# Optimization experiments

Measured on AMD Instinct MI355X. Metric: run time of the kernel, lower is better.

The kernel has to match this reference:

```python
import jax, jax.numpy as jnp
import numpy as np

P = 262144
H = 256
EPS = 1e-12  # torch F.normalize eps


def _l2norm(x):
    # matches torch.nn.functional.normalize(x, dim=-1): x / max(||x||, eps)
    n = jnp.linalg.norm(x, axis=-1, keepdims=True)
    return x / jnp.maximum(n, EPS)


def _mlp(x, params):
    # params: list of (W, b); ReLU on all but last layer
    for W, b in params[:-1]:
        x = jax.nn.relu(x @ W + b)
    W, b = params[-1]
    return x @ W + b


def setup_inputs() -> dict:
    key = jax.random.key(0)
    ks = jax.random.split(key, 24)
    inp = {
        "normals": jax.random.normal(ks[0], (P, 3), dtype=jnp.float32),
        "view_dirs": jax.random.normal(ks[1], (P, 3), dtype=jnp.float32),
        "roughness": jax.random.uniform(ks[2], (P, 1), dtype=jnp.float32),
        "r0": jax.random.uniform(ks[3], (P, 1), dtype=jnp.float32),
    }
    # diffuse MLP: 3 -> 256 -> 256 -> 256 -> 3
    d_dims = [3, H, H, H, 3]
    # specular MLP: 8 -> 256 -> 256 -> 256 -> 3
    s_dims = [8, H, H, H, 3]
    k = 4
    for i in range(4):
        fan = d_dims[i]
        inp[f"dW{i}"] = jax.random.normal(ks[k], (d_dims[i], d_dims[i + 1]), dtype=jnp.float32) * (2.0 / fan) ** 0.5
        inp[f"db{i}"] = jnp.zeros((d_dims[i + 1],), dtype=jnp.float32)
        k += 1
    for i in range(4):
        fan = s_dims[i]
        inp[f"sW{i}"] = jax.random.normal(ks[k], (s_dims[i], s_dims[i + 1]), dtype=jnp.float32) * (2.0 / fan) ** 0.5
        inp[f"sb{i}"] = jnp.zeros((s_dims[i + 1],), dtype=jnp.float32)
        k += 1
    return inp


def reference(normals, view_dirs, roughness, r0,
              dW0, db0, dW1, db1, dW2, db2, dW3, db3,
              sW0, sb0, sW1, sb1, sW2, sb2, sW3, sb3):
    n = _l2norm(normals)
    v = _l2norm(view_dirs)
    inputs_specular = jnp.concatenate((n, v, roughness, r0), axis=-1)  # [P,8]
    visible = (n * v).sum(axis=-1) > 0  # [P]
    d_params = [(dW0, db0), (dW1, db1), (dW2, db2), (dW3, db3)]
    s_params = [(sW0, sb0), (sW1, sb1), (sW2, sb2), (sW3, sb3)]
    # Faithful to gather->MLP->scatter-into-zeros: pointwise MLP computed
    # everywhere, non-visible rows zeroed (identical math, static shapes).
    mask = visible[:, None]
    diffuse_rgb = jnp.where(mask, _mlp(n, d_params), 0.0)
    specular_rgb = jnp.where(mask, _mlp(inputs_specular, s_params), 0.0)
    return (diffuse_rgb, specular_rgb)
```

## Files before the change

### kernel.cpp

```cpp
#include <hip/hip_runtime.h>

typedef _Float16 f16;
typedef _Float16 f16x8 __attribute__((ext_vector_type(8)));
typedef __fp16   fp16x2 __attribute__((ext_vector_type(2)));
typedef float    f32x16 __attribute__((ext_vector_type(16)));
typedef float    f32x4  __attribute__((ext_vector_type(4)));
typedef unsigned int u32;
typedef unsigned int u32x4 __attribute__((ext_vector_type(4)));

#define NPTS 262144

#define NET_F16   143360
#define L1_OFF    4096
#define L2_OFF    69632
#define L3_OFF    135168
#define BIAS_BYTE 573440
#define NCHUNK    70

static __device__ __forceinline__ u32 pkrtz(float a, float b) {
    fp16x2 h = __builtin_amdgcn_cvt_pkrtz(a, b);
    return __builtin_bit_cast(u32, h);
}
static __device__ __forceinline__ u32 relu_pk(float a, float b) {
    return pkrtz(fmaxf(a, 0.0f), fmaxf(b, 0.0f));
}

__global__ void prep_kernel(
    const float* __restrict__ dW0, const float* __restrict__ db0,
    const float* __restrict__ dW1, const float* __restrict__ db1,
    const float* __restrict__ dW2, const float* __restrict__ db2,
    const float* __restrict__ dW3, const float* __restrict__ db3,
    const float* __restrict__ sW0, const float* __restrict__ sb0,
    const float* __restrict__ sW1, const float* __restrict__ sb1,
    const float* __restrict__ sW2, const float* __restrict__ sb2,
    const float* __restrict__ sW3, const float* __restrict__ sb3,
    f16* __restrict__ wpk, float* __restrict__ bpk)
{
    const int ROWS = 17920;
    int t = blockIdx.x * 256 + threadIdx.x;
    if (t < 2 * ROWS) {
        int net = (t >= ROWS) ? 1 : 0;
        int r = t - net * ROWS;
        const float* W0 = net ? sW0 : dW0;
        const float* W1 = net ? sW1 : dW1;
        const float* W2 = net ? sW2 : dW2;
        const float* W3 = net ? sW3 : dW3;
        int K0 = net ? 8 : 3;
        f16* o = wpk + net * NET_F16;
        if (r < 512) {
            int lane = r & 63;
            int m  = 32 * (r >> 6) + (lane & 31);
            int kb = 8 * (lane >> 5);
            f16* q = o + r * 8;
            #pragma unroll
            for (int j = 0; j < 8; ++j) {
                int k = kb + j;
                q[j] = (f16)((k < K0) ? W0[k * 256 + m] : 0.0f);
            }
        } else if (r < 512 + 8192) {
            int rr = r - 512;
            int lane = rr & 63;
            int hh = lane >> 5;
            int m  = 32 * ((rr >> 6) & 7) + (lane & 31);
            int kt = rr >> 9;
            f16* q = o + L1_OFF + rr * 8;
            #pragma unroll
            for (int j = 0; j < 8; ++j) {
                int kp = 32 * (kt >> 1) + 16 * (kt & 1) + (j & 3) + 8 * (j >> 2) + 4 * hh;
                q[j] = (f16)W1[kp * 256 + m];
            }
        } else if (r < 512 + 16384) {
            int rr = r - (512 + 8192);
            int lane = rr & 63;
            int hh = lane >> 5;
            int m  = 32 * ((rr >> 6) & 7) + (lane & 31);
            int kt = rr >> 9;
            f16* q = o + L2_OFF + rr * 8;
            #pragma unroll
            for (int j = 0; j < 8; ++j) {
                int kp = 32 * (kt >> 1) + 16 * (kt & 1) + (j & 3) + 8 * (j >> 2) + 4 * hh;
                q[j] = (f16)W2[kp * 256 + m];
            }
        } else {
            int rr = r - (512 + 16384);
            int lane = rr & 63;
            int hh = lane >> 5;
            int m  = lane & 31;
            int kt = rr >> 6;
            f16* q = o + L3_OFF + rr * 8;
            #pragma unroll
            for (int j = 0; j < 8; ++j) {
                int kp = 32 * (kt >> 1) + 16 * (kt & 1) + (j & 3) + 8 * (j >> 2) + 4 * hh;
                q[j] = (f16)((m < 3) ? W3[kp * 3 + m] : 0.0f);
            }
        }
    } else if (t < 2 * ROWS + 1600) {
        int tb = t - 2 * ROWS;
        int net = (tb >= 800) ? 1 : 0;
        int i = tb - net * 800;
        float val;
        if (i < 768) {
            int layer = i >> 8;
            const float* bl = net ? (layer == 0 ? sb0 : layer == 1 ? sb1 : sb2)
                                  : (layer == 0 ? db0 : layer == 1 ? db1 : db2);
            int q  = i & 255;
            int rg = q & 15, h = (q >> 4) & 1;
            int m  = 32 * (q >> 5) + (rg & 3) + 8 * (rg >> 2) + 4 * h;
            val = bl[m];
        } else {
            int q  = i - 768;
            int rg = q & 15, h = q >> 4;
            int m  = (rg & 3) + 8 * (rg >> 2) + 4 * h;
            const float* b3 = net ? sb3 : db3;
            val = (m < 3) ? b3[m] : 0.0f;
        }
        bpk[net * 800 + i] = val;
    }
}

#define STAGE(S, C0, NC) do {                                                   \
    _Pragma("unroll")                                                           \
    for (int i_ = 0; i_ < (NC); ++i_) {                                         \
        const u32x4* g_ = ws + ((C0) + i_) * 512 + woff + lane;                 \
        u32x4* l_ = &ring[S][i_ * 512 + woff];                                  \
        __builtin_amdgcn_global_load_lds(                                       \
            (const __attribute__((address_space(1))) void*)g_,                  \
            (__attribute__((address_space(3))) void*)l_, 16, 0, 0);             \
        __builtin_amdgcn_global_load_lds(                                       \
            (const __attribute__((address_space(1))) void*)(g_ + 64),           \
            (__attribute__((address_space(3))) void*)(l_ + 64), 16, 0, 0);      \
    }                                                                           \
} while (0)

#define CHUNK256(S, CI, KT) do {                                                \
    const u32x4* bq_ = &ring[S][(CI) * 512];                                    \
    const f16x8 xA_ = __builtin_bit_cast(f16x8, xf0[KT]);                       \
    const f16x8 xB_ = __builtin_bit_cast(f16x8, xf1[KT]);                       \
    _Pragma("unroll")                                                           \
    for (int mt_ = 0; mt_ < 8; ++mt_) {                                         \
        const f16x8 a_ = __builtin_bit_cast(f16x8, bq_[mt_ * 64 + lane]);       \
        acc0[mt_] = __builtin_amdgcn_mfma_f32_32x32x16_f16(a_, xA_, acc0[mt_], 0, 0, 0); \
        acc1[mt_] = __builtin_amdgcn_mfma_f32_32x32x16_f16(a_, xB_, acc1[mt_], 0, 0, 0); \
    }                                                                           \
} while (0)

#define BINIT(dst, boff) do {                                                   \
    const f32x4* b4_ = (const f32x4*)(biasl + (boff) + hi * 16);                \
    const f32x4 v0_ = b4_[0], v1_ = b4_[1], v2_ = b4_[2], v3_ = b4_[3];         \
    _Pragma("unroll")                                                           \
    for (int j = 0; j < 4; ++j) {                                               \
        (dst)[j] = v0_[j]; (dst)[4 + j] = v1_[j];                               \
        (dst)[8 + j] = v2_[j]; (dst)[12 + j] = v3_[j];                          \
    }                                                                           \
} while (0)

#define EPI1(ACC, XF) do {                                                      \
    _Pragma("unroll")                                                           \
    for (int mt = 0; mt < 8; ++mt) {                                            \
        _Pragma("unroll")                                                       \
        for (int q = 0; q < 2; ++q) {                                           \
            u32x4 w;                                                            \
            w[0] = relu_pk(ACC[mt][8*q+0], ACC[mt][8*q+1]);                     \
            w[1] = relu_pk(ACC[mt][8*q+2], ACC[mt][8*q+3]);                     \
            w[2] = relu_pk(ACC[mt][8*q+4], ACC[mt][8*q+5]);                     \
            w[3] = relu_pk(ACC[mt][8*q+6], ACC[mt][8*q+7]);                     \
            XF[2*mt+q] = w;                                                     \
        }                                                                       \
    }                                                                           \
} while (0)
#define EPI() do { EPI1(acc0, xf0); EPI1(acc1, xf1); } while (0)

__launch_bounds__(256, 1)
__global__ void mlp_kernel(const float* __restrict__ gn, const float* __restrict__ gv,
                           const float* __restrict__ gro, const float* __restrict__ gr0,
                           const f16* __restrict__ wpk, const float* __restrict__ bpk,
                           float* __restrict__ out)
{
    __shared__ u32x4 ring[2][1024];
    __shared__ __align__(16) float biasl[1600];

    const int tid  = threadIdx.x;
    const int wv   = tid >> 6;
    const int lane = tid & 63;
    const int l32  = lane & 31;
    const int hi   = lane >> 5;
    const int pA   = blockIdx.x * 256 + wv * 64 + l32;
    const int pB   = pA + 32;
    const int woff = wv * 128;
    const u32x4* ws = (const u32x4*)wpk;

    biasl[tid]        = bpk[tid];
    biasl[tid + 256]  = bpk[tid + 256];
    biasl[tid + 512]  = bpk[tid + 512];
    biasl[tid + 768]  = bpk[tid + 768];
    biasl[tid + 1024] = bpk[tid + 1024];
    biasl[tid + 1280] = bpk[tid + 1280];
    if (tid < 64) biasl[tid + 1536] = bpk[tid + 1536];

    STAGE(0, 0, 1);

    u32x4 xdA = {0,0,0,0}, xsA = {0,0,0,0}, xdB = {0,0,0,0}, xsB = {0,0,0,0};
    bool visA = false, visB = false;
    if (hi == 0) {
        {
            float nx = gn[3*pA], ny = gn[3*pA+1], nz = gn[3*pA+2];
            float vx = gv[3*pA], vy = gv[3*pA+1], vz = gv[3*pA+2];
            float ro = gro[pA], rr = gr0[pA];
            float ni = 1.0f / fmaxf(sqrtf(nx*nx + ny*ny + nz*nz), 1e-12f);
            float vi = 1.0f / fmaxf(sqrtf(vx*vx + vy*vy + vz*vz), 1e-12f);
            nx *= ni; ny *= ni; nz *= ni; vx *= vi; vy *= vi; vz *= vi;
            visA = (nx*vx + ny*vy + nz*vz) > 0.0f;
            xdA[0] = pkrtz(nx, ny); xdA[1] = pkrtz(nz, 0.0f);
            xsA[0] = xdA[0];        xsA[1] = pkrtz(nz, vx);
            xsA[2] = pkrtz(vy, vz); xsA[3] = pkrtz(ro, rr);
        }
        {
            float nx = gn[3*pB], ny = gn[3*pB+1], nz = gn[3*pB+2];
            float vx = gv[3*pB], vy = gv[3*pB+1], vz = gv[3*pB+2];
            float ro = gro[pB], rr = gr0[pB];
            float ni = 1.0f / fmaxf(sqrtf(nx*nx + ny*ny + nz*nz), 1e-12f);
            float vi = 1.0f / fmaxf(sqrtf(vx*vx + vy*vy + vz*vz), 1e-12f);
            nx *= ni; ny *= ni; nz *= ni; vx *= vi; vy *= vi; vz *= vi;
            visB = (nx*vx + ny*vy + nz*vz) > 0.0f;
            xdB[0] = pkrtz(nx, ny); xdB[1] = pkrtz(nz, 0.0f);
            xsB[0] = xdB[0];        xsB[1] = pkrtz(nz, vx);
            xsB[2] = pkrtz(vy, vz); xsB[3] = pkrtz(ro, rr);
        }
    }

    f32x16 acc0[8], acc1[8];
    u32x4  xf0[16], xf1[16];
    int sp = 0;

    #pragma unroll 1
    for (int net = 0; net < 2; ++net) {
        const int cb = net * 35;
        const int bb = net * 800;
        const f16x8 xhA = __builtin_bit_cast(f16x8, net ? xsA : xdA);
        const f16x8 xhB = __builtin_bit_cast(f16x8, net ? xsB : xdB);

        __syncthreads();
        STAGE(sp ^ 1, cb + 1, 2);
        {
            const u32x4* bufq = &ring[sp][0];
            #pragma unroll
            for (int mt = 0; mt < 8; ++mt) {
                f32x16 ci;
                BINIT(ci, bb + mt * 32);
                const f16x8 a = __builtin_bit_cast(f16x8, bufq[mt * 64 + lane]);
                acc0[mt] = __builtin_amdgcn_mfma_f32_32x32x16_f16(a, xhA, ci, 0, 0, 0);
                acc1[mt] = __builtin_amdgcn_mfma_f32_32x32x16_f16(a, xhB, ci, 0, 0, 0);
            }
        }
        EPI();
        sp ^= 1;

        #pragma unroll
        for (int mt = 0; mt < 8; ++mt) { BINIT(acc0[mt], bb + 256 + mt * 32); BINIT(acc1[mt], bb + 256 + mt * 32); }
        #pragma unroll
        for (int k = 1; k <= 8; ++k) {
            __syncthreads();
            STAGE(sp ^ 1, cb + 2 * k + 1, 2);
            CHUNK256(sp, 0, 2 * k - 2);
            CHUNK256(sp, 1, 2 * k - 1);
            sp ^= 1;
        }
        EPI();

        #pragma unroll
        for (int mt = 0; mt < 8; ++mt) { BINIT(acc0[mt], bb + 512 + mt * 32); BINIT(acc1[mt], bb + 512 + mt * 32); }
        #pragma unroll
        for (int k = 9; k <= 16; ++k) {
            __syncthreads();
            STAGE(sp ^ 1, cb + 2 * k + 1, 2);
            CHUNK256(sp, 0, 2 * k - 18);
            CHUNK256(sp, 1, 2 * k - 17);
            sp ^= 1;
        }
        EPI();

        __syncthreads();
        if (net == 0) STAGE(sp ^ 1, 35, 1);
        {
            f32x16 c30, c31;
            BINIT(c30, bb + 768);
            BINIT(c31, bb + 768);
            const u32x4* bq0 = &ring[sp][0];
            const u32x4* bq1 = &ring[sp][512];
            #pragma unroll
            for (int i = 0; i < 8; ++i) {
                const f16x8 a = __builtin_bit_cast(f16x8, bq0[i * 64 + lane]);
                c30 = __builtin_amdgcn_mfma_f32_32x32x16_f16(a, __builtin_bit_cast(f16x8, xf0[i]), c30, 0, 0, 0);
                c31 = __builtin_amdgcn_mfma_f32_32x32x16_f16(a, __builtin_bit_cast(f16x8, xf1[i]), c31, 0, 0, 0);
            }
            #pragma unroll
            for (int i = 0; i < 8; ++i) {
                const f16x8 a = __builtin_bit_cast(f16x8, bq1[i * 64 + lane]);
                c30 = __builtin_amdgcn_mfma_f32_32x32x16_f16(a, __builtin_bit_cast(f16x8, xf0[8 + i]), c30, 0, 0, 0);
                c31 = __builtin_amdgcn_mfma_f32_32x32x16_f16(a, __builtin_bit_cast(f16x8, xf1[8 + i]), c31, 0, 0, 0);
            }
            if (hi == 0) {
                float* opA = out + net * (NPTS * 3) + pA * 3;
                float* opB = out + net * (NPTS * 3) + pB * 3;
                opA[0] = visA ? c30[0] : 0.0f;
                opA[1] = visA ? c30[1] : 0.0f;
                opA[2] = visA ? c30[2] : 0.0f;
                opB[0] = visB ? c31[0] : 0.0f;
                opB[1] = visB ? c31[1] : 0.0f;
                opB[2] = visB ? c31[2] : 0.0f;
            }
        }
        sp ^= 1;
    }
}

extern "C" void kernel_launch(void* const* d_in, const int* in_sizes, int n_in,
                              void* d_out, int out_size, void* d_ws, size_t ws_size,
                              hipStream_t stream)
{
    f16*   wpk = (f16*)d_ws;
    float* bpk = (float*)((char*)d_ws + BIAS_BYTE);

    prep_kernel<<<147, 256, 0, stream>>>(
        (const float*)d_in[4],  (const float*)d_in[5],
        (const float*)d_in[6],  (const float*)d_in[7],
        (const float*)d_in[8],  (const float*)d_in[9],
        (const float*)d_in[10], (const float*)d_in[11],
        (const float*)d_in[12], (const float*)d_in[13],
        (const float*)d_in[14], (const float*)d_in[15],
        (const float*)d_in[16], (const float*)d_in[17],
        (const float*)d_in[18], (const float*)d_in[19],
        wpk, bpk);

    mlp_kernel<<<1024, 256, 0, stream>>>(
        (const float*)d_in[0], (const float*)d_in[1],
        (const float*)d_in[2], (const float*)d_in[3],
        wpk, bpk, (float*)d_out);
}
```

Baseline: 179.3 us.

## Triple-buffer weight staging ring with explicit vmcnt waits and barriers

Grows the LDS weight ring from two to three stages so each chunk is prefetched two iterations ahead, and replaces __syncthreads with an explicit s_waitcnt vmcnt(N) plus s_barrier so outstanding global-to-LDS loads from later stages need not drain at each step. The net loop is fully unrolled so the ring slot indices become compile-time constants. This aims to hide weight-load latency behind the MFMA work. In exchange it uses more LDS and relies on hand-counted vmcnt values, which could break correctness if the count is wrong.

```diff
diff --git a/kernel.cpp b/kernel.cpp
--- a/kernel.cpp
+++ b/kernel.cpp
@@ -11,11 +11,7 @@
 #define NPTS 262144
 
 #define NET_F16   143360
-#define L1_OFF    4096
-#define L2_OFF    69632
-#define L3_OFF    135168
 #define BIAS_BYTE 573440
-#define NCHUNK    70
 
 static __device__ __forceinline__ u32 pkrtz(float a, float b) {
     fp16x2 h = __builtin_amdgcn_cvt_pkrtz(a, b);
@@ -63,7 +59,7 @@
             int hh = lane >> 5;
             int m  = 32 * ((rr >> 6) & 7) + (lane & 31);
             int kt = rr >> 9;
-            f16* q = o + L1_OFF + rr * 8;
+            f16* q = o + 4096 + rr * 8;
             #pragma unroll
             for (int j = 0; j < 8; ++j) {
                 int kp = 32 * (kt >> 1) + 16 * (kt & 1) + (j & 3) + 8 * (j >> 2) + 4 * hh;
@@ -75,7 +71,7 @@
             int hh = lane >> 5;
             int m  = 32 * ((rr >> 6) & 7) + (lane & 31);
             int kt = rr >> 9;
-            f16* q = o + L2_OFF + rr * 8;
+            f16* q = o + 69632 + rr * 8;
             #pragma unroll
             for (int j = 0; j < 8; ++j) {
                 int kp = 32 * (kt >> 1) + 16 * (kt & 1) + (j & 3) + 8 * (j >> 2) + 4 * hh;
@@ -87,7 +83,7 @@
             int hh = lane >> 5;
             int m  = lane & 31;
             int kt = rr >> 6;
-            f16* q = o + L3_OFF + rr * 8;
+            f16* q = o + 135168 + rr * 8;
             #pragma unroll
             for (int j = 0; j < 8; ++j) {
                 int kp = 32 * (kt >> 1) + 16 * (kt & 1) + (j & 3) + 8 * (j >> 2) + 4 * hh;
@@ -118,9 +114,26 @@
     }
 }
 
-#define STAGE(S, C0, NC) do {                                                   \
+#define WAITB(WS) do {                                                          \
+    asm volatile("s_waitcnt vmcnt(" WS ") lgkmcnt(0)" ::: "memory");            \
+    __builtin_amdgcn_sched_barrier(0);                                          \
+    __builtin_amdgcn_s_barrier();                                               \
+    __builtin_amdgcn_sched_barrier(0);                                          \
+} while (0)
+
+#define STAGE1(S, C0) do {                                                      \
+    const u32x4* g_ = ws + (C0) * 512 + woff + lane;                            \
+    u32x4* l_ = &ring[S][woff];                                                 \
+    __builtin_amdgcn_global_load_lds(                                           \
+        (const __attribute__((address_space(1))) void*)g_,                      \
+        (__attribute__((address_space(3))) void*)l_, 16, 0, 0);                 \
+    __builtin_amdgcn_global_load_lds(                                           \
+        (const __attribute__((address_space(1))) void*)(g_ + 64),               \
+        (__attribute__((address_space(3))) void*)(l_ + 64), 16, 0, 0);          \
+} while (0)
+#define STAGE2(S, C0) do {                                                      \
     _Pragma("unroll")                                                           \
-    for (int i_ = 0; i_ < (NC); ++i_) {                                         \
+    for (int i_ = 0; i_ < 2; ++i_) {                                            \
         const u32x4* g_ = ws + ((C0) + i_) * 512 + woff + lane;                 \
         u32x4* l_ = &ring[S][i_ * 512 + woff];                                  \
         __builtin_amdgcn_global_load_lds(                                       \
@@ -176,7 +189,7 @@
                            const f16* __restrict__ wpk, const float* __restrict__ bpk,
                            float* __restrict__ out)
 {
-    __shared__ u32x4 ring[2][1024];
+    __shared__ u32x4 ring[3][1024];
     __shared__ __align__(16) float biasl[1600];
 
     const int tid  = threadIdx.x;
@@ -197,7 +210,8 @@
     biasl[tid + 1280] = bpk[tid + 1280];
     if (tid < 64) biasl[tid + 1536] = bpk[tid + 1536];
 
-    STAGE(0, 0, 1);
+    STAGE1(0, 0);
+    STAGE2(1, 1);
 
     u32x4 xdA = {0,0,0,0}, xsA = {0,0,0,0}, xdB = {0,0,0,0}, xsB = {0,0,0,0};
     bool visA = false, visB = false;
@@ -230,19 +244,18 @@
 
     f32x16 acc0[8], acc1[8];
     u32x4  xf0[16], xf1[16];
-    int sp = 0;
-
-    #pragma unroll 1
+
+    #pragma unroll
     for (int net = 0; net < 2; ++net) {
         const int cb = net * 35;
         const int bb = net * 800;
         const f16x8 xhA = __builtin_bit_cast(f16x8, net ? xsA : xdA);
         const f16x8 xhB = __builtin_bit_cast(f16x8, net ? xsB : xdB);
 
-        __syncthreads();
-        STAGE(sp ^ 1, cb + 1, 2);
+        WAITB("4");
+        STAGE2(2, cb + 3);
         {
-            const u32x4* bufq = &ring[sp][0];
+            const u32x4* bufq = &ring[0][0];
             #pragma unroll
             for (int mt = 0; mt < 8; ++mt) {
                 f32x16 ci;
@@ -253,40 +266,41 @@
             }
         }
         EPI();
-        sp ^= 1;
 
         #pragma unroll
         for (int mt = 0; mt < 8; ++mt) { BINIT(acc0[mt], bb + 256 + mt * 32); BINIT(acc1[mt], bb + 256 + mt * 32); }
         #pragma unroll
-        for (int k = 1; k <= 8; ++k) {
-            __syncthreads();
-            STAGE(sp ^ 1, cb + 2 * k + 1, 2);
-            CHUNK256(sp, 0, 2 * k - 2);
-            CHUNK256(sp, 1, 2 * k - 1);
-            sp ^= 1;
+        for (int t = 1; t <= 8; ++t) {
+            WAITB("4");
+            STAGE2((t + 2) % 3, cb + 2 * t + 3);
+            CHUNK256(t % 3, 0, 2 * t - 2);
+            CHUNK256(t % 3, 1, 2 * t - 1);
         }
         EPI();
 
         #pragma unroll
         for (int mt = 0; mt < 8; ++mt) { BINIT(acc0[mt], bb + 512 + mt * 32); BINIT(acc1[mt], bb + 512 + mt * 32); }
         #pragma unroll
-        for (int k = 9; k <= 16; ++k) {
-            __syncthreads();
-            STAGE(sp ^ 1, cb + 2 * k + 1, 2);
-            CHUNK256(sp, 0, 2 * k - 18);
-            CHUNK256(sp, 1, 2 * k - 17);
-            sp ^= 1;
-        }
+        for (int t = 9; t <= 15; ++t) {
+            WAITB("4");
+            STAGE2((t + 2) % 3, cb + 2 * t + 3);
+            CHUNK256(t % 3, 0, 2 * t - 18);
+            CHUNK256(t % 3, 1, 2 * t - 17);
+        }
+        WAITB("4");
+        if (net == 0) STAGE1(0, 35);
+        CHUNK256(16 % 3, 0, 14);
+        CHUNK256(16 % 3, 1, 15);
         EPI();
 
-        __syncthreads();
-        if (net == 0) STAGE(sp ^ 1, 35, 1);
+        if (net == 0) { WAITB("2"); STAGE2(1, 36); }
+        else          { WAITB("0"); }
         {
             f32x16 c30, c31;
             BINIT(c30, bb + 768);
             BINIT(c31, bb + 768);
-            const u32x4* bq0 = &ring[sp][0];
-            const u32x4* bq1 = &ring[sp][512];
+            const u32x4* bq0 = &ring[2][0];
+            const u32x4* bq1 = &ring[2][512];
             #pragma unroll
             for (int i = 0; i < 8; ++i) {
                 const f16x8 a = __builtin_bit_cast(f16x8, bq0[i * 64 + lane]);
@@ -310,7 +324,6 @@
                 opB[2] = visB ? c31[2] : 0.0f;
             }
         }
-        sp ^= 1;
     }
 }
 
```

After: 158.1 us. 1.13x faster.

## Replace block-shared double buffer with per-wave 4-deep weight ring, no barriers

Applied to the files above, without the earlier changes.

Each wave now streams the whole weight chunk into its own private 4-slot LDS ring and waits on vmcnt rather than on block-wide __syncthreads. Previously the four waves shared one double-buffered ring and hit a barrier every chunk. The new scheme keeps three chunks in flight per wave, removing inter-wave synchronisation and deepening prefetch. The cost is four times the global/L2 traffic for weights and more LDS (128KB of staging), which may reduce occupancy. The net loop is also fully unrolled.

```diff
diff --git a/kernel.cpp b/kernel.cpp
--- a/kernel.cpp
+++ b/kernel.cpp
@@ -11,11 +11,7 @@
 #define NPTS 262144
 
 #define NET_F16   143360
-#define L1_OFF    4096
-#define L2_OFF    69632
-#define L3_OFF    135168
 #define BIAS_BYTE 573440
-#define NCHUNK    70
 
 static __device__ __forceinline__ u32 pkrtz(float a, float b) {
     fp16x2 h = __builtin_amdgcn_cvt_pkrtz(a, b);
@@ -63,7 +59,7 @@
             int hh = lane >> 5;
             int m  = 32 * ((rr >> 6) & 7) + (lane & 31);
             int kt = rr >> 9;
-            f16* q = o + L1_OFF + rr * 8;
+            f16* q = o + 4096 + rr * 8;
             #pragma unroll
             for (int j = 0; j < 8; ++j) {
                 int kp = 32 * (kt >> 1) + 16 * (kt & 1) + (j & 3) + 8 * (j >> 2) + 4 * hh;
@@ -75,7 +71,7 @@
             int hh = lane >> 5;
             int m  = 32 * ((rr >> 6) & 7) + (lane & 31);
             int kt = rr >> 9;
-            f16* q = o + L2_OFF + rr * 8;
+            f16* q = o + 69632 + rr * 8;
             #pragma unroll
             for (int j = 0; j < 8; ++j) {
                 int kp = 32 * (kt >> 1) + 16 * (kt & 1) + (j & 3) + 8 * (j >> 2) + 4 * hh;
@@ -87,7 +83,7 @@
             int hh = lane >> 5;
             int m  = lane & 31;
             int kt = rr >> 6;
-            f16* q = o + L3_OFF + rr * 8;
+            f16* q = o + 135168 + rr * 8;
             #pragma unroll
             for (int j = 0; j < 8; ++j) {
                 int kp = 32 * (kt >> 1) + 16 * (kt & 1) + (j & 3) + 8 * (j >> 2) + 4 * hh;
@@ -118,22 +114,25 @@
     }
 }
 
-#define STAGE(S, C0, NC) do {                                                   \
-    _Pragma("unroll")                                                           \
-    for (int i_ = 0; i_ < (NC); ++i_) {                                         \
-        const u32x4* g_ = ws + ((C0) + i_) * 512 + woff + lane;                 \
-        u32x4* l_ = &ring[S][i_ * 512 + woff];                                  \
+#define DMA8(G) do {                                                            \
+    const u32x4* g_ = ws + (G) * 512 + lane;                                    \
+    u32x4* l_ = &stage[wv][(G) & 3][0];                                         \
+    _Pragma("unroll")                                                           \
+    for (int i_ = 0; i_ < 8; ++i_)                                              \
         __builtin_amdgcn_global_load_lds(                                       \
-            (const __attribute__((address_space(1))) void*)g_,                  \
-            (__attribute__((address_space(3))) void*)l_, 16, 0, 0);             \
-        __builtin_amdgcn_global_load_lds(                                       \
-            (const __attribute__((address_space(1))) void*)(g_ + 64),           \
-            (__attribute__((address_space(3))) void*)(l_ + 64), 16, 0, 0);      \
-    }                                                                           \
-} while (0)
-
-#define CHUNK256(S, CI, KT) do {                                                \
-    const u32x4* bq_ = &ring[S][(CI) * 512];                                    \
+            (const __attribute__((address_space(1))) void*)(g_ + i_ * 64),      \
+            (__attribute__((address_space(3))) void*)(l_ + i_ * 64), 16, 0, 0); \
+} while (0)
+
+#define VWAIT(WS) do {                                                          \
+    asm volatile("s_waitcnt vmcnt(" WS ")" ::: "memory");                       \
+    __builtin_amdgcn_sched_barrier(0);                                          \
+} while (0)
+
+#define STEP24(G) do { DMA8((G) + 3); VWAIT("24"); } while (0)
+
+#define CH256(G, KT) do {                                                       \
+    const u32x4* bq_ = &stage[wv][(G) & 3][0];                                  \
     const f16x8 xA_ = __builtin_bit_cast(f16x8, xf0[KT]);                       \
     const f16x8 xB_ = __builtin_bit_cast(f16x8, xf1[KT]);                       \
     _Pragma("unroll")                                                           \
@@ -141,6 +140,16 @@
         const f16x8 a_ = __builtin_bit_cast(f16x8, bq_[mt_ * 64 + lane]);       \
         acc0[mt_] = __builtin_amdgcn_mfma_f32_32x32x16_f16(a_, xA_, acc0[mt_], 0, 0, 0); \
         acc1[mt_] = __builtin_amdgcn_mfma_f32_32x32x16_f16(a_, xB_, acc1[mt_], 0, 0, 0); \
+    }                                                                           \
+} while (0)
+
+#define L3C(G, HB) do {                                                         \
+    const u32x4* bq_ = &stage[wv][(G) & 3][0];                                  \
+    _Pragma("unroll")                                                           \
+    for (int i_ = 0; i_ < 8; ++i_) {                                            \
+        const f16x8 a_ = __builtin_bit_cast(f16x8, bq_[i_ * 64 + lane]);        \
+        c30 = __builtin_amdgcn_mfma_f32_32x32x16_f16(a_, __builtin_bit_cast(f16x8, xf0[(HB) + i_]), c30, 0, 0, 0); \
+        c31 = __builtin_amdgcn_mfma_f32_32x32x16_f16(a_, __builtin_bit_cast(f16x8, xf1[(HB) + i_]), c31, 0, 0, 0); \
     }                                                                           \
 } while (0)
 
@@ -176,7 +185,7 @@
                            const f16* __restrict__ wpk, const float* __restrict__ bpk,
                            float* __restrict__ out)
 {
-    __shared__ u32x4 ring[2][1024];
+    __shared__ u32x4 stage[4][4][512];
     __shared__ __align__(16) float biasl[1600];
 
     const int tid  = threadIdx.x;
@@ -186,7 +195,6 @@
     const int hi   = lane >> 5;
     const int pA   = blockIdx.x * 256 + wv * 64 + l32;
     const int pB   = pA + 32;
-    const int woff = wv * 128;
     const u32x4* ws = (const u32x4*)wpk;
 
     biasl[tid]        = bpk[tid];
@@ -196,8 +204,6 @@
     biasl[tid + 1024] = bpk[tid + 1024];
     biasl[tid + 1280] = bpk[tid + 1280];
     if (tid < 64) biasl[tid + 1536] = bpk[tid + 1536];
-
-    STAGE(0, 0, 1);
 
     u32x4 xdA = {0,0,0,0}, xsA = {0,0,0,0}, xdB = {0,0,0,0}, xsB = {0,0,0,0};
     bool visA = false, visB = false;
@@ -228,21 +234,25 @@
         }
     }
 
+    __syncthreads();
+
+    DMA8(0);
+    DMA8(1);
+    DMA8(2);
+
     f32x16 acc0[8], acc1[8];
     u32x4  xf0[16], xf1[16];
-    int sp = 0;
-
-    #pragma unroll 1
+
+    #pragma unroll
     for (int net = 0; net < 2; ++net) {
         const int cb = net * 35;
         const int bb = net * 800;
         const f16x8 xhA = __builtin_bit_cast(f16x8, net ? xsA : xdA);
         const f16x8 xhB = __builtin_bit_cast(f16x8, net ? xsB : xdB);
 
-        __syncthreads();
-        STAGE(sp ^ 1, cb + 1, 2);
+        STEP24(cb + 0);
         {
-            const u32x4* bufq = &ring[sp][0];
+            const u32x4* bufq = &stage[wv][(cb + 0) & 3][0];
             #pragma unroll
             for (int mt = 0; mt < 8; ++mt) {
                 f32x16 ci;
@@ -253,52 +263,35 @@
             }
         }
         EPI();
-        sp ^= 1;
 
         #pragma unroll
         for (int mt = 0; mt < 8; ++mt) { BINIT(acc0[mt], bb + 256 + mt * 32); BINIT(acc1[mt], bb + 256 + mt * 32); }
         #pragma unroll
-        for (int k = 1; k <= 8; ++k) {
-            __syncthreads();
-            STAGE(sp ^ 1, cb + 2 * k + 1, 2);
-            CHUNK256(sp, 0, 2 * k - 2);
-            CHUNK256(sp, 1, 2 * k - 1);
-            sp ^= 1;
+        for (int s = 1; s <= 16; ++s) {
+            STEP24(cb + s);
+            CH256(cb + s, s - 1);
         }
         EPI();
 
         #pragma unroll
         for (int mt = 0; mt < 8; ++mt) { BINIT(acc0[mt], bb + 512 + mt * 32); BINIT(acc1[mt], bb + 512 + mt * 32); }
         #pragma unroll
-        for (int k = 9; k <= 16; ++k) {
-            __syncthreads();
-            STAGE(sp ^ 1, cb + 2 * k + 1, 2);
-            CHUNK256(sp, 0, 2 * k - 18);
-            CHUNK256(sp, 1, 2 * k - 17);
-            sp ^= 1;
-        }
+        for (int s = 17; s <= 31; ++s) {
+            STEP24(cb + s);
+            CH256(cb + s, s - 17);
+        }
+        if (net == 0) { STEP24(32); } else { VWAIT("16"); }
+        CH256(cb + 32, 15);
         EPI();
 
-        __syncthreads();
-        if (net == 0) STAGE(sp ^ 1, 35, 1);
         {
             f32x16 c30, c31;
             BINIT(c30, bb + 768);
             BINIT(c31, bb + 768);
-            const u32x4* bq0 = &ring[sp][0];
-            const u32x4* bq1 = &ring[sp][512];
-            #pragma unroll
-            for (int i = 0; i < 8; ++i) {
-                const f16x8 a = __builtin_bit_cast(f16x8, bq0[i * 64 + lane]);
-                c30 = __builtin_amdgcn_mfma_f32_32x32x16_f16(a, __builtin_bit_cast(f16x8, xf0[i]), c30, 0, 0, 0);
-                c31 = __builtin_amdgcn_mfma_f32_32x32x16_f16(a, __builtin_bit_cast(f16x8, xf1[i]), c31, 0, 0, 0);
-            }
-            #pragma unroll
-            for (int i = 0; i < 8; ++i) {
-                const f16x8 a = __builtin_bit_cast(f16x8, bq1[i * 64 + lane]);
-                c30 = __builtin_amdgcn_mfma_f32_32x32x16_f16(a, __builtin_bit_cast(f16x8, xf0[8 + i]), c30, 0, 0, 0);
-                c31 = __builtin_amdgcn_mfma_f32_32x32x16_f16(a, __builtin_bit_cast(f16x8, xf1[8 + i]), c31, 0, 0, 0);
-            }
+            if (net == 0) { STEP24(33); } else { VWAIT("8"); }
+            L3C(cb + 33, 0);
+            if (net == 0) { STEP24(34); } else { VWAIT("0"); }
+            L3C(cb + 34, 8);
             if (hi == 0) {
                 float* opA = out + net * (NPTS * 3) + pA * 3;
                 float* opB = out + net * (NPTS * 3) + pB * 3;
@@ -310,7 +303,6 @@
                 opB[2] = visB ? c31[2] : 0.0f;
             }
         }
-        sp ^= 1;
     }
 }
 
```

Result: faster. 164.6 us (-8.2%).
